# Performance work log

Measured on AMD Instinct MI355X. Metric: run time of the kernel, lower is better.

Reference implementation:

```python
import jax, jax.numpy as jnp
import numpy as np
from jax import lax

N = 100000          # nodes
C = 64              # classes
E = 1600000         # edges (avg degree 16)
EPS = 1e-8
PROP_STEPS = 3
ALPHA = 0.2
GLOBAL_BETA = 0.05
MIN_ANCHOR = 0.6
RESIDUAL_SCALE = 0.15
DEGREE_BIAS = 0.25
COHERENCE_BIAS = 0.2
CLUSTERING_BIAS = 0.2
GRAPH_SCALE_BIAS = 1.0
SRC_CENTER = 0.55
SRC_SHARP = 8.0
REC_CENTER = 0.5
REC_SHARP = 8.0
ACCEPT_SHARP = 12.0
ACCEPT_THRESH = 0.0
QW = 0.7   # accept_quality_weight
MW = 0.2   # accept_margin_weight
SW = 0.1   # accept_struct_weight
LOG_C = float(np.log(C))


def _spmm(edge_src, edge_dst, w, x):
    # sparse adj @ x : out[d] = sum_{e: dst(e)=d} w[e] * x[src(e)]
    return jax.ops.segment_sum(w[:, None] * x[edge_src], edge_dst, num_segments=N)


def _cos(a, b):
    # F.cosine_similarity(dim=1, eps=1e-8), keepdims
    na = jnp.maximum(jnp.linalg.norm(a, axis=1, keepdims=True), 1e-8)
    nb = jnp.maximum(jnp.linalg.norm(b, axis=1, keepdims=True), 1e-8)
    return jnp.sum(a * b, axis=1, keepdims=True) / (na * nb)


def _confidence(state):
    mass = jnp.sum(state, axis=1, keepdims=True)                 # [N,1]
    norm = state / (mass + EPS)
    entropy = -jnp.sum(norm * jnp.log(norm + EPS), axis=1, keepdims=True)
    certainty = 1.0 - entropy / LOG_C
    mass_scale = jnp.maximum(lax.stop_gradient(jnp.mean(mass)), EPS)
    magnitude = jnp.tanh(mass / mass_scale)
    return jnp.clip(0.5 * certainty + 0.5 * magnitude, 0.0, 1.0)


def _quality(state, ctx, clustering):
    lq = jnp.clip((_cos(state, ctx) + 1.0) * 0.5, 0.0, 1.0)
    probs = state / (jnp.sum(state, axis=1, keepdims=True) + EPS)
    top2, _ = lax.top_k(probs, 2)
    margin = top2[:, :1] - top2[:, 1:2]
    return QW * lq + MW * margin + SW * clustering


def _forward(logits, edge_weight, struct_feat, edge_src, edge_dst):
    seed = jax.nn.relu(logits)
    confidence = _confidence(seed)                                # [N,1]
    global_prior = jnp.sum(confidence * seed, axis=0, keepdims=True) / \
        jnp.maximum(jnp.sum(confidence), EPS)                     # [1,C]
    anchor = jnp.clip(MIN_ANCHOR + ALPHA * confidence, 0.0, 0.995)
    uncertainty = 1.0 - confidence
    log_degree = struct_feat[:, :1]
    low_degree = jnp.clip(1.0 - log_degree, 0.0, 1.0)
    clustering = struct_feat[:, 1:2]
    low_clustering = jnp.clip(1.0 - clustering, 0.0, 1.0)
    graph_scale = jnp.clip(1.0 - jnp.mean(clustering), 0.2, 1.0)
    # gates depend only on confidence -> identical every step
    source_gate = jax.nn.sigmoid(SRC_SHARP * (confidence - SRC_CENTER))
    recipient_gate = jax.nn.sigmoid(REC_SHARP * (REC_CENTER - confidence))

    propagated = seed
    for _ in range(PROP_STEPS):
        weighted_state = source_gate * propagated
        local_num = _spmm(edge_src, edge_dst, edge_weight, weighted_state)
        local_den = jnp.maximum(_spmm(edge_src, edge_dst, edge_weight, source_gate), EPS)
        local_context = local_num / local_den
        fused = (1.0 - GLOBAL_BETA) * local_context + GLOBAL_BETA * global_prior
        agreement = jnp.clip((_cos(propagated, fused) + 1.0) * 0.5, 0.0, 1.0)
        seed_agree = jnp.clip((_cos(seed, fused) + 1.0) * 0.5, 0.0, 1.0)
        sel = jnp.clip(uncertainty + DEGREE_BIAS * low_degree +
                       COHERENCE_BIAS * seed_agree + CLUSTERING_BIAS * low_clustering, 0.0, 1.0)
        update_gate = recipient_gate * sel * agreement * (1.0 - anchor)
        residual = RESIDUAL_SCALE * GRAPH_SCALE_BIAS * graph_scale * update_gate * (fused - propagated)
        propagated = jnp.maximum(anchor * seed + (1.0 - anchor) * propagated + residual, 0.0)

    base_ctx = _spmm(edge_src, edge_dst, edge_weight, seed)
    prop_ctx = _spmm(edge_src, edge_dst, edge_weight, propagated)
    base_q = _quality(seed, base_ctx, clustering)
    prop_q = _quality(propagated, prop_ctx, clustering)
    accept = jax.nn.sigmoid(ACCEPT_SHARP * (prop_q - base_q - ACCEPT_THRESH))
    return accept * propagated + (1.0 - accept) * seed


def setup_inputs() -> dict:
    key = jax.random.key(0)
    k1, k2, k3, k4, k5 = jax.random.split(key, 5)
    return {
        "logits": jax.random.normal(k1, (N, C), dtype=jnp.float32),
        "edge_weight": jax.random.uniform(k2, (E,), dtype=jnp.float32),
        "struct_feat": jax.random.uniform(k3, (N, 2), dtype=jnp.float32),
        "edge_src": jax.random.randint(k4, (E,), 0, N, dtype=jnp.int32),
        "edge_dst": jax.random.randint(k5, (E,), 0, N, dtype=jnp.int32),
    }


def reference(logits, edge_weight, struct_feat, edge_src, edge_dst):
    return _forward(logits, edge_weight, struct_feat, edge_src, edge_dst)
```

## Files before the change

### kernel.cpp

```cpp
#include <hip/hip_runtime.h>
#include <math.h>

#define NN 100000
#define CC 64
#define EPSF 1e-8f
#define LOG_C 4.1588830833596715f
#define SCAN_BS 1024
#define NSB ((NN + SCAN_BS - 1) / SCAN_BS)

typedef unsigned short ushortT;
typedef unsigned int uintT;

__device__ __forceinline__ float waveSum(float v) {
#pragma unroll
    for (int off = 32; off; off >>= 1) v += __shfl_xor(v, off);
    return v;
}
__device__ __forceinline__ float redCSum(float v) {
    v += __shfl_xor(v, 1); v += __shfl_xor(v, 2); v += __shfl_xor(v, 4);
    return v;
}
__device__ __forceinline__ float redCMax(float v) {
    v = fmaxf(v, __shfl_xor(v, 1)); v = fmaxf(v, __shfl_xor(v, 2)); v = fmaxf(v, __shfl_xor(v, 4));
    return v;
}
__device__ __forceinline__ float redGSum(float v) {
    v += __shfl_xor(v, 8); v += __shfl_xor(v, 16); v += __shfl_xor(v, 32);
    return v;
}
__device__ __forceinline__ float clip01(float v) { return fminf(fmaxf(v, 0.f), 1.f); }
__device__ __forceinline__ float sigmoidf(float x) { return 1.f / (1.f + expf(-x)); }

__device__ __forceinline__ void unpack8(const uint4 v, float* x) {
    x[0] = __uint_as_float(v.x << 16); x[1] = __uint_as_float(v.x & 0xFFFF0000u);
    x[2] = __uint_as_float(v.y << 16); x[3] = __uint_as_float(v.y & 0xFFFF0000u);
    x[4] = __uint_as_float(v.z << 16); x[5] = __uint_as_float(v.z & 0xFFFF0000u);
    x[6] = __uint_as_float(v.w << 16); x[7] = __uint_as_float(v.w & 0xFFFF0000u);
}
__device__ __forceinline__ uintT f2bf(float f) {
    uintT u = __float_as_uint(f);
    return (u + 0x7FFFu + ((u >> 16) & 1u)) >> 16;
}
__device__ __forceinline__ uint4 pack8(const float* x) {
    uint4 o;
    o.x = f2bf(x[0]) | (f2bf(x[1]) << 16);
    o.y = f2bf(x[2]) | (f2bf(x[3]) << 16);
    o.z = f2bf(x[4]) | (f2bf(x[5]) << 16);
    o.w = f2bf(x[6]) | (f2bf(x[7]) << 16);
    return o;
}


__global__ void k_seed(const float* __restrict__ logits, const float* __restrict__ sf,
                       float* __restrict__ seedF, ushortT* __restrict__ seedH,
                       float* __restrict__ mass, float* __restrict__ cert,
                       float* __restrict__ scal) {
    int lane = threadIdx.x & 63;
    int wid = threadIdx.x >> 6;
    float accm = 0.f, accc = 0.f;
    for (int row = blockIdx.x * 4 + wid; row < NN; row += gridDim.x * 4) {
        float l = logits[row * CC + lane];
        float s = fmaxf(l, 0.f);
        seedF[row * CC + lane] = s;
        seedH[row * CC + lane] = (ushortT)f2bf(s);
        float m = waveSum(s);
        float nrm = s / (m + EPSF);
        float ent = waveSum(-nrm * logf(nrm + EPSF));
        if (lane == 0) {
            mass[row] = m;
            cert[row] = 1.f - ent / LOG_C;
            accm += m;
            accc += sf[row * 2 + 1];
        }
    }
    __shared__ float sm[8];
    if (lane == 0) { sm[wid] = accm; sm[4 + wid] = accc; }
    __syncthreads();
    if (threadIdx.x == 0) {
        atomicAdd(&scal[0], sm[0] + sm[1] + sm[2] + sm[3]);
        atomicAdd(&scal[1], sm[4] + sm[5] + sm[6] + sm[7]);
    }
}

__global__ void k_conf(const float* __restrict__ seedF, const float* __restrict__ mass,
                       const float* __restrict__ cert, float* __restrict__ conf,
                       float* __restrict__ sg, float* __restrict__ scal,
                       float* __restrict__ gp) {
    int lane = threadIdx.x & 63;
    int wid = threadIdx.x >> 6;
    float msc = fmaxf(scal[0] * (1.f / NN), EPSF);
    float accgp = 0.f, accconf = 0.f;
    for (int row = blockIdx.x * 4 + wid; row < NN; row += gridDim.x * 4) {
        float m = mass[row], ct = cert[row];
        float cf = clip01(0.5f * ct + 0.5f * tanhf(m / msc));
        accgp += cf * seedF[row * CC + lane];
        if (lane == 0) {
            conf[row] = cf;
            sg[row] = sigmoidf(8.f * (cf - 0.55f));
            accconf += cf;
        }
    }
    __shared__ float sgp[256];
    __shared__ float scf[4];
    sgp[threadIdx.x] = accgp;
    if (lane == 0) scf[wid] = accconf;
    __syncthreads();
    if (threadIdx.x < 64)
        atomicAdd(&gp[lane], sgp[lane] + sgp[64 + lane] + sgp[128 + lane] + sgp[192 + lane]);
    if (threadIdx.x == 0) atomicAdd(&scal[2], scf[0] + scf[1] + scf[2] + scf[3]);
}

__global__ void k_finalize(float* __restrict__ scal, float* __restrict__ gp) {
    float sc = fmaxf(scal[2], EPSF);
    gp[threadIdx.x] = gp[threadIdx.x] / sc;
    if (threadIdx.x == 0) {
        scal[3] = fminf(fmaxf(1.f - scal[1] * (1.f / NN), 0.2f), 1.f);
    }
}


__global__ void k_hist(const int* __restrict__ dst, int* __restrict__ count, int E) {
    int i = blockIdx.x * blockDim.x + threadIdx.x;
    int stride = gridDim.x * blockDim.x;
    for (; i < E; i += stride) atomicAdd(&count[dst[i]], 1);
}

__global__ void k_bsum(const int* __restrict__ count, int* __restrict__ bsum) {
    int b = blockIdx.x, t = threadIdx.x;
    int base = b * SCAN_BS + t * 4;
    int s = 0;
#pragma unroll
    for (int k = 0; k < 4; ++k) {
        int i = base + k;
        if (i < NN) s += count[i];
    }
#pragma unroll
    for (int off = 32; off; off >>= 1) s += __shfl_xor(s, off);
    __shared__ int red[4];
    if ((t & 63) == 0) red[t >> 6] = s;
    __syncthreads();
    if (t == 0) bsum[b] = red[0] + red[1] + red[2] + red[3];
}

__global__ void k_boff(const int* __restrict__ bsum, int* __restrict__ boff,
                       int* __restrict__ row_start) {
    int acc = 0;
    for (int i = 0; i < NSB; ++i) { boff[i] = acc; acc += bsum[i]; }
    row_start[NN] = acc;
}

__global__ void k_scanwrite(const int* __restrict__ count, const int* __restrict__ boff,
                            int* __restrict__ row_start, int* __restrict__ cursor) {
    int b = blockIdx.x, t = threadIdx.x, lane = t & 63, wid = t >> 6;
    int base = b * SCAN_BS + t * 4;
    int c0 = 0, c1 = 0, c2 = 0, c3 = 0;
    if (base < NN) c0 = count[base];
    if (base + 1 < NN) c1 = count[base + 1];
    if (base + 2 < NN) c2 = count[base + 2];
    if (base + 3 < NN) c3 = count[base + 3];
    int s = c0 + c1 + c2 + c3;
    int incl = s;
#pragma unroll
    for (int off = 1; off < 64; off <<= 1) {
        int o = __shfl_up(incl, off);
        if (lane >= off) incl += o;
    }
    __shared__ int wsum[4];
    if (lane == 63) wsum[wid] = incl;
    __syncthreads();
    int woff = 0;
    for (int i = 0; i < wid; ++i) woff += wsum[i];
    int excl = boff[b] + woff + incl - s;
    if (base < NN) { row_start[base] = excl; cursor[base] = excl; excl += c0; }
    if (base + 1 < NN) { row_start[base + 1] = excl; cursor[base + 1] = excl; excl += c1; }
    if (base + 2 < NN) { row_start[base + 2] = excl; cursor[base + 2] = excl; excl += c2; }
    if (base + 3 < NN) { row_start[base + 3] = excl; cursor[base + 3] = excl; excl += c3; }
}

__global__ void k_scatter(const int* __restrict__ src, const int* __restrict__ dst,
                          const float* __restrict__ w, int* __restrict__ cursor,
                          int2* __restrict__ edge_pk, int E) {
    int i = blockIdx.x * blockDim.x + threadIdx.x;
    int stride = gridDim.x * blockDim.x;
    for (; i < E; i += stride) {
        int d = dst[i];
        int pos = atomicAdd(&cursor[d], 1);
        edge_pk[pos] = make_int2(src[i], __float_as_int(w[i]));
    }
}


template <int MODE>
__global__ __launch_bounds__(256) void k_csr(
    const int2* __restrict__ edge_pk, const int* __restrict__ row_start,
    const ushortT* __restrict__ xH, const float* __restrict__ sg,
    const float* __restrict__ seedF, const float* __restrict__ sf,
    const float* __restrict__ conf, const float* __restrict__ gp,
    const float* __restrict__ scal, float* __restrict__ den,
    float* __restrict__ bq, ushortT* __restrict__ poutH,
    float* __restrict__ outF) {
    int lane = threadIdx.x & 63;
    int row = blockIdx.x * 4 + (threadIdx.x >> 6);
    if (row >= NN) return;
    int g = lane >> 3, c = lane & 7;
    int rs = row_start[row], re = row_start[row + 1];

    float acc[8], accn[8];
    float accden = 0.f;
#pragma unroll
    for (int i = 0; i < 8; ++i) { acc[i] = 0.f; accn[i] = 0.f; }

    for (int base = rs; base < re; base += 16) {
        int e0 = base + g;
        int e1 = base + 8 + g;
        int2 pk0 = make_int2(0, 0), pk1 = make_int2(0, 0);
        if (e0 < re) pk0 = edge_pk[e0];
        if (e1 < re) pk1 = edge_pk[e1];
        float w0 = __int_as_float(pk0.y);
        float w1 = __int_as_float(pk1.y);
        const uint4 v0 = *(const uint4*)(xH + (size_t)pk0.x * CC + c * 8);
        const uint4 v1 = *(const uint4*)(xH + (size_t)pk1.x * CC + c * 8);
        float x0[8], x1[8];
        unpack8(v0, x0);
        unpack8(v1, x1);
        float wa0 = w0, wa1 = w1;
        if (MODE == 1) { wa0 = w0 * sg[pk0.x]; wa1 = w1 * sg[pk1.x]; }
#pragma unroll
        for (int i = 0; i < 8; ++i) acc[i] += wa0 * x0[i] + wa1 * x1[i];
        if (MODE == 0) {
            float ws0 = w0 * sg[pk0.x];
            float ws1 = w1 * sg[pk1.x];
#pragma unroll
            for (int i = 0; i < 8; ++i) accn[i] += ws0 * x0[i] + ws1 * x1[i];
            accden += ws0 + ws1;
        }
    }

#pragma unroll
    for (int i = 0; i < 8; ++i) acc[i] = redGSum(acc[i]);

    if (MODE == 1) {
        float dn = fmaxf(den[row], EPSF);
        float inv = 1.f / dn;
        float p[8], s[8], g8[8], f[8];
        uint4 pv = *(const uint4*)(xH + (size_t)row * CC + c * 8);
        unpack8(pv, p);
        const float4 sa = *(const float4*)(seedF + (size_t)row * CC + c * 8);
        const float4 sb = *(const float4*)(seedF + (size_t)row * CC + c * 8 + 4);
        s[0] = sa.x; s[1] = sa.y; s[2] = sa.z; s[3] = sa.w;
        s[4] = sb.x; s[5] = sb.y; s[6] = sb.z; s[7] = sb.w;
        const float4 ga = *(const float4*)(gp + c * 8);
        const float4 gb = *(const float4*)(gp + c * 8 + 4);
        g8[0] = ga.x; g8[1] = ga.y; g8[2] = ga.z; g8[3] = ga.w;
        g8[4] = gb.x; g8[5] = gb.y; g8[6] = gb.z; g8[7] = gb.w;
        float pf = 0.f, pp = 0.f, ff = 0.f, sfv = 0.f, ss = 0.f;
#pragma unroll
        for (int i = 0; i < 8; ++i) {
            f[i] = 0.95f * (acc[i] * inv) + 0.05f * g8[i];
            pf += p[i] * f[i]; pp += p[i] * p[i]; ff += f[i] * f[i];
            sfv += s[i] * f[i]; ss += s[i] * s[i];
        }
        pf = redCSum(pf); pp = redCSum(pp); ff = redCSum(ff);
        sfv = redCSum(sfv); ss = redCSum(ss);
        float nf = fmaxf(sqrtf(ff), 1e-8f);
        float agree = clip01((pf / (fmaxf(sqrtf(pp), 1e-8f) * nf) + 1.f) * 0.5f);
        float sagree = clip01((sfv / (fmaxf(sqrtf(ss), 1e-8f) * nf) + 1.f) * 0.5f);
        float cf = conf[row];
        float anchor = fminf(fmaxf(0.6f + 0.2f * cf, 0.f), 0.995f);
        float lowdeg = clip01(1.f - sf[row * 2 + 0]);
        float lowcl = clip01(1.f - sf[row * 2 + 1]);
        float rec = sigmoidf(8.f * (0.5f - cf));
        float sel = clip01((1.f - cf) + 0.25f * lowdeg + 0.2f * sagree + 0.2f * lowcl);
        float ug = rec * sel * agree * (1.f - anchor);
        float rsc = 0.15f * scal[3] * ug;
        if (g == 0) {
            float o[8];
#pragma unroll
            for (int i = 0; i < 8; ++i)
                o[i] = fmaxf(anchor * s[i] + (1.f - anchor) * p[i] + rsc * (f[i] - p[i]), 0.f);
            *(uint4*)(poutH + (size_t)row * CC + c * 8) = pack8(o);
        }
        return;
    }

    float s[8];
    if (MODE == 0) {
        const float4 sa = *(const float4*)(seedF + (size_t)row * CC + c * 8);
        const float4 sb = *(const float4*)(seedF + (size_t)row * CC + c * 8 + 4);
        s[0] = sa.x; s[1] = sa.y; s[2] = sa.z; s[3] = sa.w;
        s[4] = sb.x; s[5] = sb.y; s[6] = sb.z; s[7] = sb.w;
    } else {
        uint4 pv = *(const uint4*)(xH + (size_t)row * CC + c * 8);
        unpack8(pv, s);
    }
    float dot = 0.f, ss = 0.f, cc2 = 0.f, m = 0.f;
#pragma unroll
    for (int i = 0; i < 8; ++i) {
        dot += s[i] * acc[i]; ss += s[i] * s[i]; cc2 += acc[i] * acc[i]; m += s[i];
    }
    dot = redCSum(dot); ss = redCSum(ss); cc2 = redCSum(cc2); m = redCSum(m);
    float cosv = dot / (fmaxf(sqrtf(ss), 1e-8f) * fmaxf(sqrtf(cc2), 1e-8f));
    float lq = clip01((cosv + 1.f) * 0.5f);
    float minv = 1.f / (m + EPSF);
    float lmax = -3.4e38f;
#pragma unroll
    for (int i = 0; i < 8; ++i) lmax = fmaxf(lmax, s[i] * minv);
    float m1 = redCMax(lmax);
    float cnt = 0.f, mlt = -3.4e38f;
#pragma unroll
    for (int i = 0; i < 8; ++i) {
        float p = s[i] * minv;
        cnt += (p == m1) ? 1.f : 0.f;
        mlt = fmaxf(mlt, (p < m1) ? p : -3.4e38f);
    }
    cnt = redCSum(cnt);
    mlt = redCMax(mlt);
    float m2 = (cnt >= 2.f) ? m1 : mlt;
    float q = 0.7f * lq + 0.2f * (m1 - m2) + 0.1f * sf[row * 2 + 1];

    if (MODE == 0) {
#pragma unroll
        for (int i = 0; i < 8; ++i) accn[i] = redGSum(accn[i]);
        accden = redGSum(accden);
        float dn = fmaxf(accden, EPSF);
        float inv = 1.f / dn;
        float g8[8], f[8];
        const float4 ga = *(const float4*)(gp + c * 8);
        const float4 gb = *(const float4*)(gp + c * 8 + 4);
        g8[0] = ga.x; g8[1] = ga.y; g8[2] = ga.z; g8[3] = ga.w;
        g8[4] = gb.x; g8[5] = gb.y; g8[6] = gb.z; g8[7] = gb.w;
        float sfv = 0.f, ff = 0.f;
#pragma unroll
        for (int i = 0; i < 8; ++i) {
            f[i] = 0.95f * (accn[i] * inv) + 0.05f * g8[i];
            sfv += s[i] * f[i]; ff += f[i] * f[i];
        }
        sfv = redCSum(sfv); ff = redCSum(ff);
        float nf = fmaxf(sqrtf(ff), 1e-8f);
        float sagree = clip01((sfv / (fmaxf(sqrtf(ss), 1e-8f) * nf) + 1.f) * 0.5f);
        float cf = conf[row];
        float anchor = fminf(fmaxf(0.6f + 0.2f * cf, 0.f), 0.995f);
        float lowdeg = clip01(1.f - sf[row * 2 + 0]);
        float lowcl = clip01(1.f - sf[row * 2 + 1]);
        float rec = sigmoidf(8.f * (0.5f - cf));
        float sel = clip01((1.f - cf) + 0.25f * lowdeg + 0.2f * sagree + 0.2f * lowcl);
        float ug = rec * sel * sagree * (1.f - anchor);
        float rsc = 0.15f * scal[3] * ug;
        if (g == 0) {
            float o[8];
#pragma unroll
            for (int i = 0; i < 8; ++i) o[i] = fmaxf(s[i] + rsc * (f[i] - s[i]), 0.f);
            *(uint4*)(poutH + (size_t)row * CC + c * 8) = pack8(o);
        }
        if (lane == 0) {
            den[row] = accden;
            bq[row] = q;
        }
    } else {
        float accp = sigmoidf(12.f * (q - bq[row]));
        const float4 sa = *(const float4*)(seedF + (size_t)row * CC + c * 8);
        const float4 sb = *(const float4*)(seedF + (size_t)row * CC + c * 8 + 4);
        float sd[8] = {sa.x, sa.y, sa.z, sa.w, sb.x, sb.y, sb.z, sb.w};
        if (g == 0) {
            float4 o1, o2;
            o1.x = accp * s[0] + (1.f - accp) * sd[0];
            o1.y = accp * s[1] + (1.f - accp) * sd[1];
            o1.z = accp * s[2] + (1.f - accp) * sd[2];
            o1.w = accp * s[3] + (1.f - accp) * sd[3];
            o2.x = accp * s[4] + (1.f - accp) * sd[4];
            o2.y = accp * s[5] + (1.f - accp) * sd[5];
            o2.z = accp * s[6] + (1.f - accp) * sd[6];
            o2.w = accp * s[7] + (1.f - accp) * sd[7];
            *(float4*)(outF + (size_t)row * CC + c * 8) = o1;
            *(float4*)(outF + (size_t)row * CC + c * 8 + 4) = o2;
        }
    }
}


extern "C" void kernel_launch(void* const* d_in, const int* in_sizes, int n_in,
                              void* d_out, int out_size, void* d_ws, size_t ws_size,
                              hipStream_t stream) {
    const float* logits = (const float*)d_in[0];
    const float* ew = (const float*)d_in[1];
    const float* sf = (const float*)d_in[2];
    const int* esrc = (const int*)d_in[3];
    const int* edst = (const int*)d_in[4];
    float* out = (float*)d_out;
    int E = in_sizes[1];

    float* ws = (float*)d_ws;
    float* seedF = ws;
    ushortT* seedH = (ushortT*)(seedF + NN * CC);
    ushortT* propAH = seedH + NN * CC;
    int2* edge_pk = (int2*)(propAH + NN * CC);
    float* fb = (float*)(edge_pk + E);
    float* massA = fb;
    float* certA = massA + NN;
    float* confA = certA + NN;
    float* sgA = confA + NN;
    float* denA = sgA + NN;
    float* bqA = denA + NN;
    float* scal = bqA + NN;
    float* gp = scal + 16;
    int* count = (int*)(gp + 64);
    int* cursor = count + NN;
    int* row_start = cursor + NN;
    int* bsum = row_start + NN + 1;
    int* boff = bsum + NSB;
    ushortT* propBH = (ushortT*)d_out;

    hipMemsetAsync(scal, 0, 16 * sizeof(float), stream);
    hipMemsetAsync(count, 0, NN * sizeof(int), stream);

    const int redBlocks = 1024;
    const int rowBlocks = (NN + 3) / 4;
    const int edgeBlocks = 1024;

    k_seed<<<redBlocks, 256, 0, stream>>>(logits, sf, seedF, seedH, massA, certA, scal);
    k_conf<<<redBlocks, 256, 0, stream>>>(seedF, massA, certA, confA, sgA, scal, gp);
    k_finalize<<<1, 64, 0, stream>>>(scal, gp);

    k_hist<<<edgeBlocks, 256, 0, stream>>>(edst, count, E);
    k_bsum<<<NSB, 256, 0, stream>>>(count, bsum);
    k_boff<<<1, 1, 0, stream>>>(bsum, boff, row_start);
    k_scanwrite<<<NSB, 256, 0, stream>>>(count, boff, row_start, cursor);
    k_scatter<<<edgeBlocks, 256, 0, stream>>>(esrc, edst, ew, cursor, edge_pk, E);

    k_csr<0><<<rowBlocks, 256, 0, stream>>>(edge_pk, row_start, seedH, sgA, seedF, sf,
                                            confA, gp, scal, denA, bqA, propAH, nullptr);
    k_csr<1><<<rowBlocks, 256, 0, stream>>>(edge_pk, row_start, propAH, sgA, seedF, sf,
                                            confA, gp, scal, denA, bqA, propBH, nullptr);
    k_csr<1><<<rowBlocks, 256, 0, stream>>>(edge_pk, row_start, propBH, sgA, seedF, sf,
                                            confA, gp, scal, denA, bqA, propAH, nullptr);
    k_csr<2><<<rowBlocks, 256, 0, stream>>>(edge_pk, row_start, propAH, sgA, seedF, sf,
                                            confA, gp, scal, denA, bqA, nullptr, out);
}
```

Before: 582.2 us.

## Replace atomic CSR scatter with two-pass region-binned counting sort

Replaces the single global-atomic scatter of edges into CSR order with a two-level binning sort. Edges are first binned into 1024-row regions using shared-memory counters and a single-block scan, then each region is unbinned into exact row positions with shared-memory atomics. This aims to swap random global atomics and scattered writes for local atomics and writes that stay within a region, at the cost of four extra kernel launches and a temporary edge buffer. The new path runs only if the workspace is large enough, otherwise it falls back to the old scatter.

```diff
diff --git a/kernel.cpp b/kernel.cpp
--- a/kernel.cpp
+++ b/kernel.cpp
@@ -7,6 +7,8 @@
 #define LOG_C 4.1588830833596715f
 #define SCAN_BS 1024
 #define NSB ((NN + SCAN_BS - 1) / SCAN_BS)
+#define NREG ((NN + 1023) >> 10)
+#define RBLK 256
 
 typedef unsigned short ushortT;
 typedef unsigned int uintT;
@@ -177,6 +179,93 @@
     if (base + 3 < NN) { row_start[base + 3] = excl; cursor[base + 3] = excl; excl += c3; }
 }
 
+
+__global__ __launch_bounds__(256) void k_rcount(const int* __restrict__ dst,
+                                                int* __restrict__ cnts, int E) {
+    __shared__ int h[NREG];
+    for (int i = threadIdx.x; i < NREG; i += 256) h[i] = 0;
+    __syncthreads();
+    int per = (E + RBLK - 1) / RBLK;
+    int b0 = blockIdx.x * per;
+    int b1 = min(b0 + per, E);
+    for (int e = b0 + threadIdx.x; e < b1; e += 256)
+        atomicAdd(&h[dst[e] >> 10], 1);
+    __syncthreads();
+    for (int r = threadIdx.x; r < NREG; r += 256)
+        cnts[r * RBLK + blockIdx.x] = h[r];
+}
+
+__global__ __launch_bounds__(1024) void k_rscan(const int* __restrict__ cnts,
+                                                int* __restrict__ offs) {
+    const int TOT = NREG * RBLK;
+    const int PER = (TOT + 1023) / 1024;
+    int t = threadIdx.x, lane = t & 63, wid = t >> 6;
+    int base = t * PER;
+    int loc[PER];
+    int s = 0;
+#pragma unroll
+    for (int k = 0; k < PER; ++k) {
+        int i = base + k;
+        int v = (i < TOT) ? cnts[i] : 0;
+        loc[k] = s;
+        s += v;
+    }
+    int incl = s;
+#pragma unroll
+    for (int off = 1; off < 64; off <<= 1) {
+        int o = __shfl_up(incl, off);
+        if (lane >= off) incl += o;
+    }
+    __shared__ int wsum[16];
+    if (lane == 63) wsum[wid] = incl;
+    __syncthreads();
+    int woff = 0;
+    for (int i = 0; i < wid; ++i) woff += wsum[i];
+    int excl = woff + incl - s;
+#pragma unroll
+    for (int k = 0; k < PER; ++k) {
+        int i = base + k;
+        if (i < TOT) offs[i] = excl + loc[k];
+    }
+}
+
+__global__ __launch_bounds__(256) void k_rbin(const int* __restrict__ src,
+                                              const int* __restrict__ dst,
+                                              const float* __restrict__ w,
+                                              const int* __restrict__ offs,
+                                              int2* __restrict__ tmp_pk, int E) {
+    __shared__ int cur[NREG];
+    for (int r = threadIdx.x; r < NREG; r += 256)
+        cur[r] = offs[r * RBLK + blockIdx.x];
+    __syncthreads();
+    int per = (E + RBLK - 1) / RBLK;
+    int b0 = blockIdx.x * per;
+    int b1 = min(b0 + per, E);
+    for (int e = b0 + threadIdx.x; e < b1; e += 256) {
+        int d = dst[e];
+        int r = d >> 10;
+        int pos = atomicAdd(&cur[r], 1);
+        tmp_pk[pos] = make_int2(src[e] | ((d & 1023) << 17), __float_as_int(w[e]));
+    }
+}
+
+__global__ __launch_bounds__(256) void k_runbin(const int* __restrict__ row_start,
+                                                const int2* __restrict__ tmp_pk,
+                                                int2* __restrict__ edge_pk) {
+    __shared__ int cur[1024];
+    int r0 = blockIdx.x << 10;
+    int r1 = min(r0 + 1024, NN);
+    for (int i = threadIdx.x; i < r1 - r0; i += 256) cur[i] = row_start[r0 + i];
+    __syncthreads();
+    int s = row_start[r0], e = row_start[r1];
+    for (int i = s + threadIdx.x; i < e; i += 256) {
+        int2 t = tmp_pk[i];
+        int dl = (t.x >> 17) & 1023;
+        int pos = atomicAdd(&cur[dl], 1);
+        edge_pk[pos] = make_int2(t.x & 0x1FFFF, t.y);
+    }
+}
+
 __global__ void k_scatter(const int* __restrict__ src, const int* __restrict__ dst,
                           const float* __restrict__ w, int* __restrict__ cursor,
                           int2* __restrict__ edge_pk, int E) {
@@ -394,7 +483,8 @@
     ushortT* seedH = (ushortT*)(seedF + NN * CC);
     ushortT* propAH = seedH + NN * CC;
     int2* edge_pk = (int2*)(propAH + NN * CC);
-    float* fb = (float*)(edge_pk + E);
+    int2* tmp_pk = edge_pk + E;
+    float* fb = (float*)(tmp_pk + E);
     float* massA = fb;
     float* certA = massA + NN;
     float* confA = certA + NN;
@@ -408,7 +498,12 @@
     int* row_start = cursor + NN;
     int* bsum = row_start + NN + 1;
     int* boff = bsum + NSB;
+    int* cnts = boff + NSB;
+    int* offs = cnts + NREG * RBLK;
     ushortT* propBH = (ushortT*)d_out;
+
+    size_t need_bytes = (size_t)((char*)(offs + NREG * RBLK) - (char*)ws);
+    bool sort_path = ws_size >= need_bytes;
 
     hipMemsetAsync(scal, 0, 16 * sizeof(float), stream);
     hipMemsetAsync(count, 0, NN * sizeof(int), stream);
@@ -425,7 +520,15 @@
     k_bsum<<<NSB, 256, 0, stream>>>(count, bsum);
     k_boff<<<1, 1, 0, stream>>>(bsum, boff, row_start);
     k_scanwrite<<<NSB, 256, 0, stream>>>(count, boff, row_start, cursor);
-    k_scatter<<<edgeBlocks, 256, 0, stream>>>(esrc, edst, ew, cursor, edge_pk, E);
+
+    if (sort_path) {
+        k_rcount<<<RBLK, 256, 0, stream>>>(edst, cnts, E);
+        k_rscan<<<1, 1024, 0, stream>>>(cnts, offs);
+        k_rbin<<<RBLK, 256, 0, stream>>>(esrc, edst, ew, offs, tmp_pk, E);
+        k_runbin<<<NREG, 256, 0, stream>>>(row_start, tmp_pk, edge_pk);
+    } else {
+        k_scatter<<<edgeBlocks, 256, 0, stream>>>(esrc, edst, ew, cursor, edge_pk, E);
+    }
 
     k_csr<0><<<rowBlocks, 256, 0, stream>>>(edge_pk, row_start, seedH, sgA, seedF, sf,
                                             confA, gp, scal, denA, bqA, propAH, nullptr);
```

Result: faster. 528.1 us (-9.3%).
